# Kernel tuning notes

Hardware: AMD Instinct MI355X
Metric: run time of the kernel (lower is better)

Reference implementation:

```python
import jax, jax.numpy as jnp
import numpy as np

B, C, H, W = 8, 512, 64, 64
NH, D = 8, 64            # num_heads, head_dim (C = NH*D)
WH, WW = 8, 8            # window size
EPS = 1e-5
SCALE = D ** -0.5


def _layernorm(x, g, b):
    mu = jnp.mean(x, axis=-1, keepdims=True)
    var = jnp.mean((x - mu) ** 2, axis=-1, keepdims=True)
    return (x - mu) * jax.lax.rsqrt(var + EPS) * g + b


def _rope_cache(n, d):
    pos = jnp.arange(n, dtype=jnp.float32)
    inv_freq = 1.0 / (10000.0 ** (jnp.arange(0, d, 2, dtype=jnp.float32) / d))
    sinusoid = pos[:, None] * inv_freq[None, :]          # (n, d//2)
    return jnp.stack([jnp.sin(sinusoid), jnp.cos(sinusoid)], axis=-1).reshape(n, d)


def _apply_rope(x, rope):
    # x: (B, nH, N, d); rope: (N, d) packed [sin, cos] interleaved
    b, nh, n, d = x.shape
    x_ = x.reshape(b, nh, n, d // 2, 2)
    r = rope.reshape(n, d // 2, 2)
    sin, cos = r[..., 0], r[..., 1]                      # (N, d//2)
    x0, x1 = x_[..., 0], x_[..., 1]
    xr0 = x0 * cos - x1 * sin
    xr1 = x0 * sin + x1 * cos
    return jnp.stack([xr0, xr1], axis=-1).reshape(b, nh, n, d)


def _relative_index(wh, ww):
    ch, cw = np.meshgrid(np.arange(wh), np.arange(ww), indexing='ij')
    flat = np.stack([ch.reshape(-1), cw.reshape(-1)])    # (2, Ws)
    rel = flat[:, :, None] - flat[:, None, :]            # (2, Ws, Ws)
    rel = rel.transpose(1, 2, 0).astype(np.int64)
    rel[..., 0] += wh - 1
    rel[..., 1] += ww - 1
    rel[..., 0] *= 2 * ww - 1
    return jnp.asarray(rel.sum(-1))                      # (Ws, Ws)


def setup_inputs() -> dict:
    key = jax.random.key(0)
    ks = jax.random.split(key, 12)
    s = 0.02
    table_size = (2 * WH - 1) * (2 * WW - 1)
    return {
        'q':  jax.random.normal(ks[0], (B, C, H, W), jnp.float32),
        'kv': jax.random.normal(ks[1], (B, C, H, W), jnp.float32),
        'g_q':  jnp.ones((C,), jnp.float32),  'b_q_ln':  jnp.zeros((C,), jnp.float32),
        'g_kv': jnp.ones((C,), jnp.float32),  'b_kv_ln': jnp.zeros((C,), jnp.float32),
        'Wq': jax.random.normal(ks[2], (C, C), jnp.float32) * s, 'bq': jnp.zeros((C,), jnp.float32),
        'Wk': jax.random.normal(ks[3], (C, C), jnp.float32) * s, 'bk': jnp.zeros((C,), jnp.float32),
        'Wv': jax.random.normal(ks[4], (C, C), jnp.float32) * s, 'bv': jnp.zeros((C,), jnp.float32),
        'Wo': jax.random.normal(ks[5], (C, C), jnp.float32) * s, 'bo': jnp.zeros((C,), jnp.float32),
        'bias_table': jax.random.normal(ks[6], (table_size, NH), jnp.float32) * s,
    }


def reference(q, kv, g_q, b_q_ln, g_kv, b_kv_ln, Wq, bq, Wk, bk, Wv, bv, Wo, bo, bias_table):
    N = H * W
    Hn, Wn = H // WH, W // WW
    nw = Hn * Wn
    Ws = WH * WW

    # flatten NCHW -> (B, N, C)
    q_seq = q.reshape(B, C, N).transpose(0, 2, 1)
    kv_seq = kv.reshape(B, C, N).transpose(0, 2, 1)
    q_seq = _layernorm(q_seq, g_q, b_q_ln)
    kv_seq = _layernorm(kv_seq, g_kv, b_kv_ln)

    Q = (q_seq @ Wq.T + bq).reshape(B, N, NH, D).transpose(0, 2, 1, 3)   # (B,nH,N,d)
    K = (kv_seq @ Wk.T + bk).reshape(B, N, NH, D).transpose(0, 2, 1, 3)
    V = (kv_seq @ Wv.T + bv).reshape(B, N, NH, D).transpose(0, 2, 1, 3)

    rope = _rope_cache(N, D)
    Q = _apply_rope(Q, rope)
    K = _apply_rope(K, rope)

    # window partition: (B,nH,H,W,d) -> (nH, B*nw, Ws, d); head-major to match torch cat order
    def part(x):
        x = x.reshape(B, NH, Hn, WH, Wn, WW, D)
        return x.transpose(1, 0, 2, 4, 3, 5, 6).reshape(NH, B * nw, Ws, D)

    Qw, Kw, Vw = part(Q), part(K), part(V)

    attn = jnp.einsum('hnqd,hnkd->hnqk', Qw, Kw) * SCALE                 # (nH, B*nw, Ws, Ws)
    rel_idx = _relative_index(WH, WW)
    bias = bias_table[rel_idx.reshape(-1)].reshape(Ws, Ws, NH).transpose(2, 0, 1)  # (nH, Ws, Ws)
    attn = attn + bias[:, None, :, :]
    attn = jax.nn.softmax(attn, axis=-1)
    out_w = jnp.einsum('hnqk,hnkd->hnqd', attn, Vw)                      # (nH, B*nw, Ws, d)

    # window reverse + head concat -> (B, N, C)
    out = out_w.reshape(NH, B, Hn, Wn, WH, WW, D)
    out = out.transpose(1, 2, 4, 3, 5, 0, 6).reshape(B, N, NH * D)

    out = out @ Wo.T + bo
    out = out + q_seq                                                    # residual w/ normed q (as in source)
    return out.transpose(0, 2, 1).reshape(B, C, H, W)
```

## Files before the change

### kernel.cpp

```cpp
#include <hip/hip_runtime.h>


typedef unsigned short u16;
typedef __bf16 bf16x8 __attribute__((ext_vector_type(8)));
typedef float f32x4 __attribute__((ext_vector_type(4)));
typedef u16 u16x8 __attribute__((ext_vector_type(8)));
typedef u16 u16x4 __attribute__((ext_vector_type(4)));

__device__ __forceinline__ u16 f2bf(float f) {
    __bf16 h = (__bf16)f;
    return __builtin_bit_cast(u16, h);
}
__device__ __forceinline__ float bf2f(u16 u) {
    return (float)__builtin_bit_cast(__bf16, u);
}
__device__ __forceinline__ f32x4 mfma16(bf16x8 a, bf16x8 b, f32x4 c) {
    return __builtin_amdgcn_mfma_f32_16x16x32_bf16(a, b, c, 0, 0, 0);
}
__device__ __forceinline__ void gl_lds16(const u16* g, u16* l) {
    __builtin_amdgcn_global_load_lds((const __attribute__((address_space(1))) void*)g,
                                     (__attribute__((address_space(3))) void*)l, 16, 0, 0);
}
__device__ __forceinline__ int swapb(int n) {
    return (n & 0xE07) | ((n & 0x1C0) >> 3) | ((n & 0x038) << 3);
}

__global__ __launch_bounds__(256) void setup_kernel(
    const float* __restrict__ Wq, const float* __restrict__ Wk,
    const float* __restrict__ Wv, const float* __restrict__ Wo,
    const float* __restrict__ btab,
    u16* __restrict__ wq, u16* __restrict__ wk,
    u16* __restrict__ wv, u16* __restrict__ wo,
    float* __restrict__ rope, float* __restrict__ biasf)
{
    int idx = blockIdx.x * 256 + threadIdx.x;
    {
        int w = idx >> 18, e = idx & 262143;
        const float* src = (w == 0) ? Wq : (w == 1) ? Wk : (w == 2) ? Wv : Wo;
        u16* dst = (w == 0) ? wq : (w == 1) ? wk : (w == 2) ? wv : wo;
        dst[e] = f2bf(src[e]);
    }
    if (idx < 131072) {
        int n = idx >> 5, j = idx & 31;
        float inv = powf(10000.0f, -(float)j / 32.0f);
        float a = (float)n * inv;
        float s, c;
        sincosf(a, &s, &c);
        rope[n * 64 + 2 * j] = s;
        rope[n * 64 + 2 * j + 1] = c;
    }
    if (idx < 32768) {
        int q = idx & 63, pp = (idx >> 6) & 63, h = idx >> 12;
        int r1 = pp >> 3, c1 = pp & 7, r2 = q >> 3, c2 = q & 7;
        int ri = (r1 - r2 + 7) * 15 + (c1 - c2 + 7);
        biasf[idx] = btab[ri * 8 + h];
    }
}

__global__ __launch_bounds__(256) void ln_kernel(
    const float* __restrict__ x, const float* __restrict__ g,
    const float* __restrict__ be, u16* __restrict__ out)
{
    __shared__ u16 sX[512 * 36];
    __shared__ float sS[1024];
    __shared__ float sQ[1024];
    __shared__ float sMu[32], sInv[32];

    const int tid = threadIdx.x;
    const int b = blockIdx.x >> 7, grp = blockIdx.x & 127;
    const int nbase = grp << 5;
    const int t4 = tid & 7;
    const int cg = tid >> 3;

    const float* xp = x + ((size_t)b << 21) + nbase + (t4 << 2);
    float sm[4] = {0.f, 0.f, 0.f, 0.f}, sq2[4] = {0.f, 0.f, 0.f, 0.f};
#pragma unroll 4
    for (int it = 0; it < 16; it++) {
        int c = (it << 5) + cg;
        f32x4 v = *(const f32x4*)&xp[(size_t)c << 12];
        u16x4 h;
#pragma unroll
        for (int r = 0; r < 4; r++) {
            sm[r] += v[r];
            sq2[r] += v[r] * v[r];
            h[r] = f2bf(v[r]);
        }
        *(u16x4*)&sX[c * 36 + (t4 << 2)] = h;
    }
#pragma unroll
    for (int r = 0; r < 4; r++) {
        sS[tid * 4 + r] = sm[r];
        sQ[tid * 4 + r] = sq2[r];
    }
    __syncthreads();
    if (tid < 32) {
        int t4v = tid >> 2, r = tid & 3;
        float a = 0.f, q2 = 0.f;
#pragma unroll
        for (int c2 = 0; c2 < 32; c2++) {
            int i2 = ((c2 << 3) + t4v) * 4 + r;
            a += sS[i2];
            q2 += sQ[i2];
        }
        float mu = a * (1.f / 512.f);
        float var = q2 * (1.f / 512.f) - mu * mu;
        sMu[tid] = mu;
        sInv[tid] = rsqrtf(var + 1e-5f);
    }
    __syncthreads();

    const int t = tid >> 3;
    const int cs = (tid & 7) << 3;
    float mu = sMu[t], inv = sInv[t];
    int p = swapb(nbase + t);
    size_t orow = ((size_t)((b << 12) + p)) * 512;
#pragma unroll
    for (int it = 0; it < 8; it++) {
        int c0 = cs + (it << 6);
        f32x4 g0 = *(const f32x4*)&g[c0];
        f32x4 g1 = *(const f32x4*)&g[c0 + 4];
        f32x4 e0 = *(const f32x4*)&be[c0];
        f32x4 e1 = *(const f32x4*)&be[c0 + 4];
        u16x8 o;
#pragma unroll
        for (int k = 0; k < 8; k++) {
            float v = bf2f(sX[(c0 + k) * 36 + t]);
            float gg = (k < 4) ? g0[k] : g1[k - 4];
            float bb = (k < 4) ? e0[k] : e1[k - 4];
            o[k] = f2bf((v - mu) * inv * gg + bb);
        }
        *(u16x8*)&out[orow + c0] = o;
    }
}

__global__ __launch_bounds__(256) void gemm_qkv(
    const u16* __restrict__ qn, const u16* __restrict__ kvn,
    const u16* __restrict__ wq, const u16* __restrict__ wk, const u16* __restrict__ wv,
    const float* __restrict__ bq, const float* __restrict__ bk, const float* __restrict__ bv,
    const float* __restrict__ rope,
    u16* __restrict__ Qr, u16* __restrict__ Kr, u16* __restrict__ VT)
{
    __shared__ u16 sA[128 * 32];
    __shared__ u16 sB[128 * 32];
    __shared__ u16 sU[9216];

    const int kind = blockIdx.y >> 2;
    const int n0 = (blockIdx.y & 3) * 128;
    const u16* A = (kind == 0) ? qn : kvn;
    const u16* W = (kind == 0) ? wq : (kind == 1) ? wk : wv;
    const float* bias = (kind == 0) ? bq : (kind == 1) ? bk : bv;

    const int m0 = blockIdx.x * 128;
    const int tid = threadIdx.x;
    const int lane = tid & 63, wave = tid >> 6;
    const int ln = lane & 15, lq = lane >> 4;
    const int wm = wave & 1, wn = wave >> 1;

    const int srow = wave * 16 + (lane >> 2);
    const int sseg = (lane & 3) << 3;
    const u16* gA0 = A + (size_t)(m0 + srow) * 512 + sseg;
    const u16* gA1 = gA0 + (size_t)64 * 512;
    const u16* gB0 = W + (size_t)(n0 + srow) * 512 + sseg;
    const u16* gB1 = gB0 + (size_t)64 * 512;
    u16* lA0 = &sA[wave * 16 * 32];
    u16* lA1 = &sA[(64 + wave * 16) * 32];
    u16* lB0 = &sB[wave * 16 * 32];
    u16* lB1 = &sB[(64 + wave * 16) * 32];

    f32x4 acc[4][4] = {};

    for (int kt = 0; kt < 512; kt += 32) {
        gl_lds16(gA0 + kt, lA0);
        gl_lds16(gA1 + kt, lA1);
        gl_lds16(gB0 + kt, lB0);
        gl_lds16(gB1 + kt, lB1);
        __syncthreads();
        bf16x8 af[4], bfr[4];
#pragma unroll
        for (int i = 0; i < 4; i++)
            af[i] = *(const bf16x8*)&sA[(wm * 64 + i * 16 + ln) * 32 + lq * 8];
#pragma unroll
        for (int j = 0; j < 4; j++)
            bfr[j] = *(const bf16x8*)&sB[(wn * 64 + j * 16 + ln) * 32 + lq * 8];
#pragma unroll
        for (int i = 0; i < 4; i++)
#pragma unroll
            for (int j = 0; j < 4; j++)
                acc[i][j] = mfma16(af[i], bfr[j], acc[i][j]);
        __syncthreads();
    }

    float bj[4];
#pragma unroll
    for (int j = 0; j < 4; j++) bj[j] = bias[n0 + wn * 64 + j * 16 + ln];

    if (kind < 2) {
        u16* Out = (kind == 0) ? Qr : Kr;
#pragma unroll
        for (int half = 0; half < 2; half++) {
            __syncthreads();
            if (wm == half) {
#pragma unroll
                for (int i = 0; i < 4; i++)
#pragma unroll
                    for (int j = 0; j < 4; j++)
#pragma unroll
                        for (int r = 0; r < 4; r++)
                            sU[(i * 16 + lq * 4 + r) * 136 + wn * 64 + j * 16 + ln] =
                                f2bf(acc[i][j][r] + bj[j]);
            }
            __syncthreads();
#pragma unroll
            for (int it = 0; it < 4; it++) {
                int idx = it * 256 + tid;
                int row = idx >> 4;
                int cseg = (idx & 15) * 8;
                u16x8 v = *(const u16x8*)&sU[row * 136 + cseg];
                int t = m0 + half * 64 + row;
                int n = swapb(t & 4095);
                float f[8];
#pragma unroll
                for (int k = 0; k < 8; k++) f[k] = bf2f(v[k]);
                {
                    int d0 = cseg & 63;
                    const float* rp = &rope[n * 64 + d0];
                    f32x4 r0 = *(const f32x4*)rp;
                    f32x4 r1 = *(const f32x4*)(rp + 4);
#pragma unroll
                    for (int pp = 0; pp < 4; pp++) {
                        float sn = (pp < 2) ? r0[2 * pp] : r1[2 * (pp - 2)];
                        float cs2 = (pp < 2) ? r0[2 * pp + 1] : r1[2 * (pp - 2) + 1];
                        float x0 = f[2 * pp], x1 = f[2 * pp + 1];
                        f[2 * pp] = x0 * cs2 - x1 * sn;
                        f[2 * pp + 1] = x0 * sn + x1 * cs2;
                    }
                }
                u16x8 o;
#pragma unroll
                for (int k = 0; k < 8; k++) o[k] = f2bf(f[k]);
                *(u16x8*)&Out[(size_t)t * 512 + n0 + cseg] = o;
            }
        }
    } else {
        const int wq0 = m0 & 4095;
        const int bb = m0 >> 12;
#pragma unroll
        for (int half = 0; half < 2; half++) {
            __syncthreads();
            if (wm == half) {
#pragma unroll
                for (int i = 0; i < 4; i++)
#pragma unroll
                    for (int j = 0; j < 4; j++) {
                        u16x4 pk;
#pragma unroll
                        for (int r = 0; r < 4; r++) pk[r] = f2bf(acc[i][j][r] + bj[j]);
                        *(u16x4*)&sU[(wn * 64 + j * 16 + ln) * 72 + i * 16 + lq * 4] = pk;
                    }
            }
            __syncthreads();
#pragma unroll
            for (int ii = 0; ii < 4; ii++) {
                int idx = ii * 256 + tid;
                int col = idx >> 3, ch = (idx & 7) << 3;
                u16x8 v = *(const u16x8*)&sU[col * 72 + ch];
                int c = n0 + col;
                int hh = c >> 6, dd = c & 63;
                *(u16x8*)&VT[((size_t)((((bb << 3) + hh) << 6) + dd)) * 4096 +
                             wq0 + half * 64 + ch] = v;
            }
        }
    }
}

__global__ __launch_bounds__(256) void gemm_out(
    const u16* __restrict__ A, const u16* __restrict__ Bw,
    const float* __restrict__ bias, const u16* __restrict__ qn,
    float* __restrict__ Out)
{
    __shared__ u16 sA[128 * 32];
    __shared__ u16 sB[128 * 32];
    __shared__ u16 sR[128 * 136];

    const int m0 = blockIdx.x * 128;
    const int n0 = blockIdx.y * 128;
    const int tid = threadIdx.x;
    const int lane = tid & 63, wave = tid >> 6;
    const int ln = lane & 15, lq = lane >> 4;
    const int wm = wave & 1, wn = wave >> 1;

    const int srow = wave * 16 + (lane >> 2);
    const int sseg = (lane & 3) << 3;
    const u16* gA0 = A + (size_t)(m0 + srow) * 512 + sseg;
    const u16* gA1 = gA0 + (size_t)64 * 512;
    const u16* gB0 = Bw + (size_t)(n0 + srow) * 512 + sseg;
    const u16* gB1 = gB0 + (size_t)64 * 512;
    u16* lA0 = &sA[wave * 16 * 32];
    u16* lA1 = &sA[(64 + wave * 16) * 32];
    u16* lB0 = &sB[wave * 16 * 32];
    u16* lB1 = &sB[(64 + wave * 16) * 32];

    f32x4 acc[4][4] = {};

    for (int kt = 0; kt < 512; kt += 32) {
        gl_lds16(gA0 + kt, lA0);
        gl_lds16(gA1 + kt, lA1);
        gl_lds16(gB0 + kt, lB0);
        gl_lds16(gB1 + kt, lB1);
        __syncthreads();
        bf16x8 af[4], bfr[4];
#pragma unroll
        for (int i = 0; i < 4; i++)
            af[i] = *(const bf16x8*)&sA[(wm * 64 + i * 16 + ln) * 32 + lq * 8];
#pragma unroll
        for (int j = 0; j < 4; j++)
            bfr[j] = *(const bf16x8*)&sB[(wn * 64 + j * 16 + ln) * 32 + lq * 8];
#pragma unroll
        for (int i = 0; i < 4; i++)
#pragma unroll
            for (int j = 0; j < 4; j++)
                acc[i][j] = mfma16(af[i], bfr[j], acc[i][j]);
        __syncthreads();
    }

#pragma unroll
    for (int it = 0; it < 8; it++) {
        int idx = it * 256 + tid;
        int row = idx >> 4, c8 = (idx & 15) << 3;
        *(u16x8*)&sR[row * 136 + c8] = *(const u16x8*)&qn[(size_t)(m0 + row) * 512 + n0 + c8];
    }
    __syncthreads();

    int cj[4];
    float bj[4];
#pragma unroll
    for (int j = 0; j < 4; j++) {
        cj[j] = n0 + wn * 64 + j * 16 + ln;
        bj[j] = bias[cj[j]];
    }
#pragma unroll
    for (int i = 0; i < 4; i++) {
        int t0 = m0 + wm * 64 + i * 16 + lq * 4;
        int bb = t0 >> 12;
        int nb = swapb(t0 & 4095);
        int lrow = wm * 64 + i * 16 + lq * 4;
#pragma unroll
        for (int j = 0; j < 4; j++) {
            int lcol = wn * 64 + j * 16 + ln;
            f32x4 v;
#pragma unroll
            for (int r = 0; r < 4; r++)
                v[r] = acc[i][j][r] + bj[j] + bf2f(sR[(lrow + r) * 136 + lcol]);
            *(f32x4*)&Out[((size_t)((bb << 9) + cj[j]) << 12) + nb] = v;
        }
    }
}

__global__ __launch_bounds__(256) void attn_kernel(
    const u16* __restrict__ Q, const u16* __restrict__ K, const u16* __restrict__ VT,
    const float* __restrict__ biasf, u16* __restrict__ Out)
{
    __shared__ u16 sQ[64 * 72];
    __shared__ u16 sK[64 * 72];
    __shared__ u16 sVT[64 * 72];
    __shared__ u16 sP[4][16 * 72];

    const int tid = threadIdx.x;
    const int h = blockIdx.x & 7;
    const int w = (blockIdx.x >> 3) & 63;
    const int b = blockIdx.x >> 9;
    const int lane = tid & 63, wave = tid >> 6;
    const int ln = lane & 15, lq = lane >> 4;

    const size_t qrow0 = (size_t)(b << 12) + w * 64;
    const size_t vrow0 = ((size_t)(((b << 3) + h) << 6)) * 4096 + w * 64;

#pragma unroll
    for (int ii = 0; ii < 2; ii++) {
        int idx = ii * 256 + tid;
        int row = idx >> 3, ch = (idx & 7) << 3;
        size_t ga = (qrow0 + row) * 512 + h * 64 + ch;
        *(u16x8*)&sQ[row * 72 + ch] = *(const u16x8*)&Q[ga];
        *(u16x8*)&sK[row * 72 + ch] = *(const u16x8*)&K[ga];
        *(u16x8*)&sVT[row * 72 + ch] = *(const u16x8*)&VT[vrow0 + (size_t)row * 4096 + ch];
    }
    __syncthreads();

    f32x4 s[4] = {};
#pragma unroll
    for (int ks = 0; ks < 2; ks++) {
        bf16x8 a = *(const bf16x8*)&sQ[(wave * 16 + ln) * 72 + ks * 32 + lq * 8];
#pragma unroll
        for (int j = 0; j < 4; j++) {
            bf16x8 bb = *(const bf16x8*)&sK[(j * 16 + ln) * 72 + ks * 32 + lq * 8];
            s[j] = mfma16(a, bb, s[j]);
        }
    }

    float sv[4][4];
#pragma unroll
    for (int r = 0; r < 4; r++) {
        const float* bp = &biasf[((h * 64 + wave * 16 + lq * 4 + r) << 6) + ln];
#pragma unroll
        for (int j = 0; j < 4; j++) sv[r][j] = s[j][r] * 0.125f + bp[j * 16];
    }
#pragma unroll
    for (int r = 0; r < 4; r++) {
        float m = fmaxf(fmaxf(sv[r][0], sv[r][1]), fmaxf(sv[r][2], sv[r][3]));
        m = fmaxf(m, __shfl_xor(m, 1));
        m = fmaxf(m, __shfl_xor(m, 2));
        m = fmaxf(m, __shfl_xor(m, 4));
        m = fmaxf(m, __shfl_xor(m, 8));
        float sum = 0.f;
#pragma unroll
        for (int j = 0; j < 4; j++) {
            sv[r][j] = __expf(sv[r][j] - m);
            sum += sv[r][j];
        }
        sum += __shfl_xor(sum, 1);
        sum += __shfl_xor(sum, 2);
        sum += __shfl_xor(sum, 4);
        sum += __shfl_xor(sum, 8);
        float rinv = 1.f / sum;
#pragma unroll
        for (int j = 0; j < 4; j++)
            sP[wave][(lq * 4 + r) * 72 + j * 16 + ln] = f2bf(sv[r][j] * rinv);
    }

    f32x4 o[4] = {};
#pragma unroll
    for (int ks = 0; ks < 2; ks++) {
        bf16x8 a = *(const bf16x8*)&sP[wave][ln * 72 + ks * 32 + lq * 8];
#pragma unroll
        for (int jd = 0; jd < 4; jd++) {
            bf16x8 bb = *(const bf16x8*)&sVT[(jd * 16 + ln) * 72 + ks * 32 + lq * 8];
            o[jd] = mfma16(a, bb, o[jd]);
        }
    }

#pragma unroll
    for (int r = 0; r < 4; r++)
#pragma unroll
        for (int jd = 0; jd < 4; jd++)
            sQ[(wave * 16 + lq * 4 + r) * 72 + jd * 16 + ln] = f2bf(o[jd][r]);
    __syncthreads();
#pragma unroll
    for (int ii = 0; ii < 2; ii++) {
        int idx = ii * 256 + tid;
        int row = idx >> 3, ch = (idx & 7) << 3;
        *(u16x8*)&Out[(qrow0 + row) * 512 + h * 64 + ch] = *(const u16x8*)&sQ[row * 72 + ch];
    }
}

extern "C" void kernel_launch(void* const* d_in, const int* in_sizes, int n_in,
                              void* d_out, int out_size, void* d_ws, size_t ws_size,
                              hipStream_t stream)
{
    const float* q    = (const float*)d_in[0];
    const float* kv   = (const float*)d_in[1];
    const float* g_q  = (const float*)d_in[2];
    const float* b_q  = (const float*)d_in[3];
    const float* g_kv = (const float*)d_in[4];
    const float* b_kv = (const float*)d_in[5];
    const float* Wq   = (const float*)d_in[6];
    const float* bq   = (const float*)d_in[7];
    const float* Wk   = (const float*)d_in[8];
    const float* bk   = (const float*)d_in[9];
    const float* Wv   = (const float*)d_in[10];
    const float* bv   = (const float*)d_in[11];
    const float* Wo   = (const float*)d_in[12];
    const float* bo   = (const float*)d_in[13];
    const float* btab = (const float*)d_in[14];

    char* ws = (char*)d_ws;
    u16* qn      = (u16*)(ws);
    u16* kvn     = (u16*)(ws + 33554432);
    u16* VT      = (u16*)(ws + 67108864);
    float* rope  = (float*)(ws + 100663296);
    float* biasf = (float*)(ws + 101711872);
    u16* wq      = (u16*)(ws + 101842944);
    u16* wk      = (u16*)(ws + 102367232);
    u16* wv      = (u16*)(ws + 102891520);
    u16* wo      = (u16*)(ws + 103415808);
    u16* aout    = kvn;
    u16* Qr      = (u16*)d_out;
    u16* Kr      = Qr + 16777216;

    setup_kernel<<<4096, 256, 0, stream>>>(Wq, Wk, Wv, Wo, btab, wq, wk, wv, wo, rope, biasf);
    ln_kernel<<<1024, 256, 0, stream>>>(q, g_q, b_q, qn);
    ln_kernel<<<1024, 256, 0, stream>>>(kv, g_kv, b_kv, kvn);
    gemm_qkv<<<dim3(256, 12), 256, 0, stream>>>(qn, kvn, wq, wk, wv, bq, bk, bv, rope, Qr, Kr, VT);
    attn_kernel<<<4096, 256, 0, stream>>>(Qr, Kr, VT, biasf, aout);
    gemm_out<<<dim3(256, 4), 256, 0, stream>>>(aout, wo, bo, qn, (float*)d_out);
}
```

Baseline: 367.6 us.

## Rewrite QKV GEMM as 256x256-tile double-buffered pipeline with swizzled LDS

The QKV projection GEMM moves from 128x128 tiles with a single LDS buffer and a full sync per k-step to 256x256 tiles on 512 threads. Global-to-LDS loads are double-buffered and issued two k-steps ahead with explicit vmcnt waits, split-phase barriers and raised MFMA priority. LDS reads use an XOR-swizzled layout to avoid bank conflicts, and a block-index remap changes the order tiles are scheduled for cache locality. The epilogues are adapted to the larger tile. This gives more data reuse and overlaps memory with compute, at the cost of higher register pressure and more fragile hand-scheduled synchronization.

```diff
diff --git a/kernel.cpp b/kernel.cpp
--- a/kernel.cpp
+++ b/kernel.cpp
@@ -133,90 +133,156 @@
     }
 }
 
-__global__ __launch_bounds__(256) void gemm_qkv(
+__global__ __launch_bounds__(512, 2) void gemm_qkv(
     const u16* __restrict__ qn, const u16* __restrict__ kvn,
     const u16* __restrict__ wq, const u16* __restrict__ wk, const u16* __restrict__ wv,
     const float* __restrict__ bq, const float* __restrict__ bk, const float* __restrict__ bv,
     const float* __restrict__ rope,
     u16* __restrict__ Qr, u16* __restrict__ Kr, u16* __restrict__ VT)
 {
-    __shared__ u16 sA[128 * 32];
-    __shared__ u16 sB[128 * 32];
-    __shared__ u16 sU[9216];
-
-    const int kind = blockIdx.y >> 2;
-    const int n0 = (blockIdx.y & 3) * 128;
-    const u16* A = (kind == 0) ? qn : kvn;
+    __shared__ __align__(16) u16 smem[32768];
+
+    const int bid = blockIdx.x;
+    const int swz = (bid & 7) * 96 + (bid >> 3);
+    const int kind = swz >> 8;
+    const int rem = swz & 255;
+    const int n0 = (rem >> 7) << 8;
+    const int m0 = (rem & 127) << 8;
+
+    const u16* Asrc = (kind == 0) ? qn : kvn;
     const u16* W = (kind == 0) ? wq : (kind == 1) ? wk : wv;
     const float* bias = (kind == 0) ? bq : (kind == 1) ? bk : bv;
 
-    const int m0 = blockIdx.x * 128;
     const int tid = threadIdx.x;
-    const int lane = tid & 63, wave = tid >> 6;
+    const int lane = tid & 63, wid = tid >> 6;
     const int ln = lane & 15, lq = lane >> 4;
-    const int wm = wave & 1, wn = wave >> 1;
-
-    const int srow = wave * 16 + (lane >> 2);
-    const int sseg = (lane & 3) << 3;
-    const u16* gA0 = A + (size_t)(m0 + srow) * 512 + sseg;
-    const u16* gA1 = gA0 + (size_t)64 * 512;
-    const u16* gB0 = W + (size_t)(n0 + srow) * 512 + sseg;
-    const u16* gB1 = gB0 + (size_t)64 * 512;
-    u16* lA0 = &sA[wave * 16 * 32];
-    u16* lA1 = &sA[(64 + wave * 16) * 32];
-    u16* lB0 = &sB[wave * 16 * 32];
-    u16* lB1 = &sB[(64 + wave * 16) * 32];
-
-    f32x4 acc[4][4] = {};
-
-    for (int kt = 0; kt < 512; kt += 32) {
-        gl_lds16(gA0 + kt, lA0);
-        gl_lds16(gA1 + kt, lA1);
-        gl_lds16(gB0 + kt, lB0);
-        gl_lds16(gB1 + kt, lB1);
-        __syncthreads();
-        bf16x8 af[4], bfr[4];
-#pragma unroll
-        for (int i = 0; i < 4; i++)
-            af[i] = *(const bf16x8*)&sA[(wm * 64 + i * 16 + ln) * 32 + lq * 8];
-#pragma unroll
-        for (int j = 0; j < 4; j++)
-            bfr[j] = *(const bf16x8*)&sB[(wn * 64 + j * 16 + ln) * 32 + lq * 8];
-#pragma unroll
-        for (int i = 0; i < 4; i++)
-#pragma unroll
-            for (int j = 0; j < 4; j++)
-                acc[i][j] = mfma16(af[i], bfr[j], acc[i][j]);
-        __syncthreads();
+    const int wr = wid >> 2, wc = wid & 3;
+
+    const int rr = tid >> 2;
+    const int cc = (tid & 3) ^ ((tid >> 3) & 3);
+    const u16* aSt = Asrc + (size_t)(m0 + rr) * 512 + cc * 8;
+    const u16* bSt = W + (size_t)(n0 + rr) * 512 + cc * 8;
+    const int aD = wid * 512;
+
+    gl_lds16(aSt, &smem[aD]);
+    gl_lds16(aSt + (size_t)128 * 512, &smem[4096 + aD]);
+    gl_lds16(bSt, &smem[16384 + aD]);
+    gl_lds16(bSt + (size_t)128 * 512, &smem[16384 + 4096 + aD]);
+    gl_lds16(aSt + 32, &smem[8192 + aD]);
+    gl_lds16(aSt + 32 + (size_t)128 * 512, &smem[8192 + 4096 + aD]);
+    gl_lds16(bSt + 32, &smem[16384 + 8192 + aD]);
+    gl_lds16(bSt + 32 + (size_t)128 * 512, &smem[16384 + 8192 + 4096 + aD]);
+
+    const int swzc = lq ^ ((ln >> 1) & 3);
+    const int aRd = (wr * 128 + ln) * 32 + swzc * 8;
+    const int bRd = 16384 + (wc * 64 + ln) * 32 + swzc * 8;
+
+    f32x4 acc[8][4] = {};
+
+    asm volatile("s_waitcnt vmcnt(4)" ::: "memory");
+    __builtin_amdgcn_s_barrier();
+    __builtin_amdgcn_sched_barrier(0);
+
+    for (int kt = 0; kt < 16; ++kt) {
+        const int slot = (kt & 1) * 8192;
+        bf16x8 bB[4];
+        {
+            f32x4 a0 = *(const f32x4*)&smem[slot + aRd];
+            f32x4 a1 = *(const f32x4*)&smem[slot + aRd + 512];
+            f32x4 a2 = *(const f32x4*)&smem[slot + aRd + 1024];
+            f32x4 a3 = *(const f32x4*)&smem[slot + aRd + 1536];
+            f32x4 b0 = *(const f32x4*)&smem[slot + bRd];
+            f32x4 b1 = *(const f32x4*)&smem[slot + bRd + 512];
+            f32x4 b2 = *(const f32x4*)&smem[slot + bRd + 1024];
+            f32x4 b3 = *(const f32x4*)&smem[slot + bRd + 1536];
+            asm volatile("" ::"v"(a0), "v"(a1), "v"(a2), "v"(a3),
+                             "v"(b0), "v"(b1), "v"(b2), "v"(b3));
+            __builtin_amdgcn_s_barrier();
+            __builtin_amdgcn_sched_barrier(0);
+            if (kt < 14) {
+                const u16* gp = bSt + (size_t)(kt + 2) * 32;
+                gl_lds16(gp, &smem[16384 + slot + aD]);
+                gl_lds16(gp + (size_t)128 * 512, &smem[16384 + slot + 4096 + aD]);
+            }
+            bf16x8 bA[4] = {__builtin_bit_cast(bf16x8, a0), __builtin_bit_cast(bf16x8, a1),
+                            __builtin_bit_cast(bf16x8, a2), __builtin_bit_cast(bf16x8, a3)};
+            bB[0] = __builtin_bit_cast(bf16x8, b0);
+            bB[1] = __builtin_bit_cast(bf16x8, b1);
+            bB[2] = __builtin_bit_cast(bf16x8, b2);
+            bB[3] = __builtin_bit_cast(bf16x8, b3);
+            __builtin_amdgcn_s_setprio(1);
+#pragma unroll
+            for (int i = 0; i < 4; ++i)
+#pragma unroll
+                for (int j = 0; j < 4; ++j)
+                    acc[i][j] = mfma16(bA[i], bB[j], acc[i][j]);
+            __builtin_amdgcn_s_setprio(0);
+        }
+        __builtin_amdgcn_sched_barrier(0);
+        __builtin_amdgcn_s_barrier();
+        __builtin_amdgcn_sched_barrier(0);
+        {
+            f32x4 h0 = *(const f32x4*)&smem[slot + aRd + 2048];
+            f32x4 h1 = *(const f32x4*)&smem[slot + aRd + 2560];
+            f32x4 h2 = *(const f32x4*)&smem[slot + aRd + 3072];
+            f32x4 h3 = *(const f32x4*)&smem[slot + aRd + 3584];
+            asm volatile("" ::"v"(h0), "v"(h1), "v"(h2), "v"(h3));
+            __builtin_amdgcn_s_barrier();
+            __builtin_amdgcn_sched_barrier(0);
+            if (kt < 14) {
+                const u16* gp = aSt + (size_t)(kt + 2) * 32;
+                gl_lds16(gp, &smem[slot + aD]);
+                gl_lds16(gp + (size_t)128 * 512, &smem[slot + 4096 + aD]);
+            }
+            bf16x8 hA[4] = {__builtin_bit_cast(bf16x8, h0), __builtin_bit_cast(bf16x8, h1),
+                            __builtin_bit_cast(bf16x8, h2), __builtin_bit_cast(bf16x8, h3)};
+            __builtin_amdgcn_s_setprio(1);
+#pragma unroll
+            for (int i = 0; i < 4; ++i)
+#pragma unroll
+                for (int j = 0; j < 4; ++j)
+                    acc[i + 4][j] = mfma16(hA[i], bB[j], acc[i + 4][j]);
+            __builtin_amdgcn_s_setprio(0);
+        }
+        if (kt < 14) {
+            asm volatile("s_waitcnt vmcnt(4)" ::: "memory");
+        } else {
+            asm volatile("s_waitcnt vmcnt(0)" ::: "memory");
+        }
+        __builtin_amdgcn_s_barrier();
+        __builtin_amdgcn_sched_barrier(0);
     }
 
     float bj[4];
 #pragma unroll
-    for (int j = 0; j < 4; j++) bj[j] = bias[n0 + wn * 64 + j * 16 + ln];
+    for (int j = 0; j < 4; ++j) bj[j] = bias[n0 + wc * 64 + j * 16 + ln];
+
+    u16* sU = smem;
 
     if (kind < 2) {
         u16* Out = (kind == 0) ? Qr : Kr;
 #pragma unroll
-        for (int half = 0; half < 2; half++) {
+        for (int g = 0; g < 4; ++g) {
             __syncthreads();
-            if (wm == half) {
-#pragma unroll
-                for (int i = 0; i < 4; i++)
-#pragma unroll
-                    for (int j = 0; j < 4; j++)
-#pragma unroll
-                        for (int r = 0; r < 4; r++)
-                            sU[(i * 16 + lq * 4 + r) * 136 + wn * 64 + j * 16 + ln] =
-                                f2bf(acc[i][j][r] + bj[j]);
+            if (wr == (g >> 1)) {
+                const int i0 = (g & 1) * 4;
+#pragma unroll
+                for (int di = 0; di < 4; ++di)
+#pragma unroll
+                    for (int j = 0; j < 4; ++j)
+#pragma unroll
+                        for (int r = 0; r < 4; ++r)
+                            sU[(di * 16 + lq * 4 + r) * 264 + wc * 64 + j * 16 + ln] =
+                                f2bf(acc[i0 + di][j][r] + bj[j]);
             }
             __syncthreads();
 #pragma unroll
-            for (int it = 0; it < 4; it++) {
-                int idx = it * 256 + tid;
-                int row = idx >> 4;
-                int cseg = (idx & 15) * 8;
-                u16x8 v = *(const u16x8*)&sU[row * 136 + cseg];
-                int t = m0 + half * 64 + row;
+            for (int it = 0; it < 4; ++it) {
+                int idx = it * 512 + tid;
+                int row = idx >> 5;
+                int cseg = (idx & 31) << 3;
+                u16x8 v = *(const u16x8*)&sU[row * 264 + cseg];
+                int t = m0 + g * 64 + row;
                 int n = swapb(t & 4095);
                 float f[8];
 #pragma unroll
@@ -245,29 +311,29 @@
         const int wq0 = m0 & 4095;
         const int bb = m0 >> 12;
 #pragma unroll
-        for (int half = 0; half < 2; half++) {
+        for (int g = 0; g < 4; ++g) {
             __syncthreads();
-            if (wm == half) {
-#pragma unroll
-                for (int i = 0; i < 4; i++)
-#pragma unroll
-                    for (int j = 0; j < 4; j++) {
+            if (wc == g) {
+#pragma unroll
+                for (int i = 0; i < 8; ++i)
+#pragma unroll
+                    for (int j = 0; j < 4; ++j) {
                         u16x4 pk;
 #pragma unroll
-                        for (int r = 0; r < 4; r++) pk[r] = f2bf(acc[i][j][r] + bj[j]);
-                        *(u16x4*)&sU[(wn * 64 + j * 16 + ln) * 72 + i * 16 + lq * 4] = pk;
+                        for (int r = 0; r < 4; ++r) pk[r] = f2bf(acc[i][j][r] + bj[j]);
+                        *(u16x4*)&sU[(j * 16 + ln) * 264 + wr * 128 + i * 16 + lq * 4] = pk;
                     }
             }
             __syncthreads();
 #pragma unroll
-            for (int ii = 0; ii < 4; ii++) {
-                int idx = ii * 256 + tid;
-                int col = idx >> 3, ch = (idx & 7) << 3;
-                u16x8 v = *(const u16x8*)&sU[col * 72 + ch];
-                int c = n0 + col;
+            for (int it = 0; it < 4; ++it) {
+                int idx = it * 512 + tid;
+                int col = idx >> 5;
+                int ch = (idx & 31) << 3;
+                u16x8 v = *(const u16x8*)&sU[col * 264 + ch];
+                int c = n0 + g * 64 + col;
                 int hh = c >> 6, dd = c & 63;
-                *(u16x8*)&VT[((size_t)((((bb << 3) + hh) << 6) + dd)) * 4096 +
-                             wq0 + half * 64 + ch] = v;
+                *(u16x8*)&VT[((size_t)((((bb << 3) + hh) << 6) + dd)) * 4096 + wq0 + ch] = v;
             }
         }
     }
@@ -489,7 +555,7 @@
     setup_kernel<<<4096, 256, 0, stream>>>(Wq, Wk, Wv, Wo, btab, wq, wk, wv, wo, rope, biasf);
     ln_kernel<<<1024, 256, 0, stream>>>(q, g_q, b_q, qn);
     ln_kernel<<<1024, 256, 0, stream>>>(kv, g_kv, b_kv, kvn);
-    gemm_qkv<<<dim3(256, 12), 256, 0, stream>>>(qn, kvn, wq, wk, wv, bq, bk, bv, rope, Qr, Kr, VT);
+    gemm_qkv<<<768, 512, 0, stream>>>(qn, kvn, wq, wk, wv, bq, bk, bv, rope, Qr, Kr, VT);
     attn_kernel<<<4096, 256, 0, stream>>>(Qr, Kr, VT, biasf, aout);
     gemm_out<<<dim3(256, 4), 256, 0, stream>>>(aout, wo, bo, qn, (float*)d_out);
 }
```

After: 354.2 us. 3.6% less time.
